# Kernel tuning notes

Hardware: AMD Instinct MI355X
Metric: run time of the kernel (lower is better)

The kernel has to match this reference:

```python
import jax, jax.numpy as jnp
import numpy as np
from jax import lax

B, S, I, H, O = 128, 1024, 512, 1024, 512


def setup_inputs() -> dict:
    key = jax.random.key(0)
    ks = jax.random.split(key, 7)
    scale_ih = 1.0 / np.sqrt(H)  # torch nn.RNN init scale
    return {
        "x": jax.random.normal(ks[0], (B, S, I), dtype=jnp.float32),
        "W_ih": jax.random.uniform(ks[1], (H, I), jnp.float32, -scale_ih, scale_ih),
        "W_hh": jax.random.uniform(ks[2], (H, H), jnp.float32, -scale_ih, scale_ih),
        "b_ih": jax.random.uniform(ks[3], (H,), jnp.float32, -scale_ih, scale_ih),
        "b_hh": jax.random.uniform(ks[4], (H,), jnp.float32, -scale_ih, scale_ih),
        "W_fc": jax.random.uniform(ks[5], (O, H), jnp.float32, -scale_ih, scale_ih),
        "b_fc": jax.random.uniform(ks[6], (O,), jnp.float32, -scale_ih, scale_ih),
    }


def reference(x, W_ih, W_hh, b_ih, b_hh, W_fc, b_fc):
    # Precompute input projections for all timesteps in one big GEMM: [B,S,H]
    xp = jnp.einsum("bsi,hi->bsh", x, W_ih) + b_ih + b_hh
    h0 = jnp.zeros((x.shape[0], W_hh.shape[0]), dtype=x.dtype)

    def step(h, xt):  # h: [B,H], xt: [B,H]
        h_new = jnp.tanh(xt + h @ W_hh.T)
        return h_new, None

    hT, _ = lax.scan(step, h0, jnp.swapaxes(xp, 0, 1))  # scan over seq dim
    # fc applied to last timestep's hidden state only
    return hT @ W_fc.T + b_fc
```

## Files before the change

### kernel.cpp

```cpp
#include <hip/hip_runtime.h>
#include <stdint.h>
#include <stddef.h>
#include <math.h>

#define B_ 128
#define S_ 1024
#define I_ 512
#define H_ 1024
#define O_ 512

typedef __attribute__((ext_vector_type(4))) float f32x4;
typedef __attribute__((ext_vector_type(8))) short short8;
typedef __attribute__((ext_vector_type(2))) unsigned int uint2v;
typedef __attribute__((ext_vector_type(4))) unsigned int uint4v;

__device__ __forceinline__ unsigned short f2bf(float f) {
    unsigned u = __builtin_bit_cast(unsigned, f);
    u += 0x7fffu + ((u >> 16) & 1u);
    return (unsigned short)(u >> 16);
}
__device__ __forceinline__ uint2v pack4(f32x4 v) {
    uint2v r;
    r.x = (unsigned)f2bf(v.x) | ((unsigned)f2bf(v.y) << 16);
    r.y = (unsigned)f2bf(v.z) | ((unsigned)f2bf(v.w) << 16);
    return r;
}
__device__ __forceinline__ unsigned long long ld_u64_coh(const unsigned long long* p) {
    return __hip_atomic_load(p, __ATOMIC_RELAXED, __HIP_MEMORY_SCOPE_AGENT);
}
__device__ __forceinline__ void st_u32_coh(unsigned int* p, unsigned int v) {
    __hip_atomic_store(p, v, __ATOMIC_RELAXED, __HIP_MEMORY_SCOPE_AGENT);
}
__device__ __forceinline__ unsigned int ld_u32_coh(const unsigned int* p) {
    return __hip_atomic_load(p, __ATOMIC_RELAXED, __HIP_MEMORY_SCOPE_AGENT);
}

#define OFF_WFI  2097152UL
#define OFF_HBUF 3145728UL
#define OFF_CNT  3670016UL
#define WS_NEED  (OFF_CNT + 2048UL)

__global__ void rnn_init(unsigned int* hb32, unsigned int* cnt) {
    int idx = blockIdx.x * 256 + threadIdx.x;
    hb32[idx] = 0u;
    hb32[idx + 65536] = 0u;
    if (blockIdx.x < 2) cnt[blockIdx.x * 256 + threadIdx.x] = 0u;
}

__global__ void rnn_convw_hh(const float* __restrict__ Whh,
                             unsigned short* __restrict__ wfh) {
    int G = blockIdx.x * 256 + threadIdx.x;
    int l = G & 63, rest = G >> 6;
    int kc = rest & 31, t = (rest >> 5) & 1, wgn = rest >> 6;
    int n  = wgn * 32 + t * 16 + (l & 15);
    int k0 = kc * 32 + (l >> 4) * 8;
    const float* src = Whh + (size_t)n * H_ + k0;
    f32x4 f0 = *(const f32x4*)src, f1 = *(const f32x4*)(src + 4);
    uint2v a = pack4(f0), b = pack4(f1);
    uint4v pk; pk.x = a.x; pk.y = a.y; pk.z = b.x; pk.w = b.y;
    *(uint4v*)(wfh + (size_t)G * 8) = pk;
}

__global__ void rnn_convw_ih(const float* __restrict__ Wih,
                             unsigned short* __restrict__ wfi) {
    int G = blockIdx.x * 256 + threadIdx.x;
    int l = G & 63, rest = G >> 6;
    int kc2 = rest & 15, t = (rest >> 4) & 1, wgn = rest >> 5;
    int n  = wgn * 32 + t * 16 + (l & 15);
    int k0 = kc2 * 32 + (l >> 4) * 8;
    const float* src = Wih + (size_t)n * I_ + k0;
    f32x4 f0 = *(const f32x4*)src, f1 = *(const f32x4*)(src + 4);
    uint2v a = pack4(f0), b = pack4(f1);
    uint4v pk; pk.x = a.x; pk.y = a.y; pk.z = b.x; pk.w = b.y;
    *(uint4v*)(wfi + (size_t)G * 8) = pk;
}

__global__ __launch_bounds__(256, 1) void rnn_rec(
    const float* __restrict__ x,
    const unsigned short* __restrict__ wfh,
    const unsigned short* __restrict__ wfi,
    const float* __restrict__ bih, const float* __restrict__ bhh,
    unsigned short* __restrict__ hbuf,
    unsigned int* __restrict__ cnt)
{
    __shared__ unsigned short ldsX[8192];
    __shared__ float red[512];

    int g = blockIdx.x & 7, wgn = blockIdx.x >> 3;
    int tid = threadIdx.x, l = tid & 63, w = tid >> 6;
    int t = w & 1, kk = w >> 1;
    int li = l & 15, q = l >> 4;

    short8 wh[16], wi[8];
    #pragma unroll
    for (int c = 0; c < 16; ++c)
        wh[c] = *(const short8*)(wfh +
            ((size_t)((wgn * 2 + t) * 32 + kk * 16 + c)) * 512 + l * 8);
    #pragma unroll
    for (int c = 0; c < 8; ++c)
        wi[c] = *(const short8*)(wfi +
            ((size_t)((wgn * 2 + t) * 16 + kk * 8 + c)) * 512 + l * 8);

    int hcol = wgn * 32 + t * 16 + li;
    float bias = 0.f;
    if (kk == 0) bias = bih[hcol] + bhh[hcol];
    int q2 = (hcol >> 3) & 3, j2 = hcol & 7;
    unsigned int* flg = cnt + g * 64;

    {
        f32x4 xr[8];
        #pragma unroll
        for (int i = 0; i < 4; ++i) {
            int G = tid + i * 256, l2 = G & 63, kc2 = G >> 6;
            const float* src = x + ((size_t)(g * 16 + (l2 & 15)) * S_ + 0) * I_
                                 + kc2 * 32 + (l2 >> 4) * 8;
            xr[2 * i]     = *(const f32x4*)src;
            xr[2 * i + 1] = *(const f32x4*)(src + 4);
        }
        #pragma unroll
        for (int i = 0; i < 4; ++i) {
            int G = tid + i * 256;
            uint2v a = pack4(xr[2 * i]), b = pack4(xr[2 * i + 1]);
            uint4v pk; pk.x = a.x; pk.y = a.y; pk.z = b.x; pk.w = b.y;
            *(uint4v*)&ldsX[(size_t)G * 8] = pk;
        }
    }
    __syncthreads();

    int bail = 0;
    #pragma unroll 1
    for (int s = 0; s < S_; ++s) {
        int cur = s & 1, nxt = cur ^ 1;
        int havex = (s + 1 < S_);

        const unsigned long long* hsrc = (const unsigned long long*)hbuf
            + (size_t)cur * 32768 + (size_t)g * 4096
            + (size_t)kk * 2048 + (size_t)l * 2;
        unsigned long long h0[16], h1[16];
        #pragma unroll
        for (int c = 0; c < 16; ++c) {
            h0[c] = ld_u64_coh(hsrc + (size_t)c * 128);
            h1[c] = ld_u64_coh(hsrc + (size_t)c * 128 + 1);
        }

        f32x4 xr[8];
        if (havex) {
            #pragma unroll
            for (int i = 0; i < 4; ++i) {
                int G = tid + i * 256, l2 = G & 63, kc2 = G >> 6;
                const float* src = x + ((size_t)(g * 16 + (l2 & 15)) * S_ + (s + 1)) * I_
                                     + kc2 * 32 + (l2 >> 4) * 8;
                xr[2 * i]     = *(const f32x4*)src;
                xr[2 * i + 1] = *(const f32x4*)(src + 4);
            }
        }

        f32x4 acc2 = {0.f, 0.f, 0.f, 0.f};
        #pragma unroll
        for (int c = 0; c < 8; ++c) {
            short8 a = *(const short8*)&ldsX[(kk * 8 + c) * 512 + l * 8];
            acc2 = __builtin_amdgcn_mfma_f32_16x16x32_bf16(a, wi[c], acc2, 0, 0, 0);
        }
        f32x4 acc = {0.f, 0.f, 0.f, 0.f};
        #pragma unroll
        for (int c = 0; c < 16; ++c) {
            union { unsigned long long qw[2]; short8 v; } u;
            u.qw[0] = h0[c]; u.qw[1] = h1[c];
            acc = __builtin_amdgcn_mfma_f32_16x16x32_bf16(u.v, wh[c], acc, 0, 0, 0);
        }
        acc += acc2;

        if (kk == 1) *(f32x4*)&red[t * 256 + l * 4] = acc;
        __syncthreads();
        if (kk == 0) {
            f32x4 p = *(const f32x4*)&red[t * 256 + l * 4];
            unsigned int* hout32 = (unsigned int*)(hbuf
                + (size_t)nxt * 131072 + (size_t)g * 16384
                + (size_t)wgn * 512 + j2);
            #pragma unroll
            for (int i = 0; i < 4; ++i) {
                float v = tanhf(acc[i] + p[i] + bias);
                unsigned short mybf = f2bf(v);
                unsigned nb = (unsigned)__shfl_xor((int)mybf, 1, 64) & 0xffffu;
                if ((li & 1) == 0) {
                    unsigned word = (unsigned)mybf | (nb << 16);
                    st_u32_coh(hout32 + (q2 * 16 + q * 4 + i) * 4, word);
                }
            }
        }
        __syncthreads();

        if (havex) {
            if (tid == 0) st_u32_coh(flg + wgn, (unsigned)(s + 1));
            #pragma unroll
            for (int i = 0; i < 4; ++i) {
                int G = tid + i * 256;
                uint2v a = pack4(xr[2 * i]), b2 = pack4(xr[2 * i + 1]);
                uint4v pk; pk.x = a.x; pk.y = a.y; pk.z = b2.x; pk.w = b2.y;
                *(uint4v*)&ldsX[(size_t)G * 8] = pk;
            }
            if (tid < 64 && !bail) {
                unsigned target = (unsigned)(s + 1);
                int polls = 0;
                while (true) {
                    unsigned v = ld_u32_coh(flg + (l & 31));
                    if (__ballot((int)(v >= target)) == ~0ull) break;
                    __builtin_amdgcn_s_sleep(1);
                    if (++polls > (1 << 22)) { bail = 1; break; }
                }
            }
            __syncthreads();
        }
    }
}

__global__ __launch_bounds__(256) void rnn_fc(
    const unsigned short* __restrict__ hb0,
    const float* __restrict__ Wfc, const float* __restrict__ bfc,
    float* __restrict__ out)
{
    __shared__ unsigned short ldsB[8 * 64 * 8];
    int n_blk = blockIdx.x;
    int tid = threadIdx.x, l = tid & 63, w = tid >> 6;
    int li = l & 15, q = l >> 4;
    f32x4 acc[8][2];
    f32x4 z = {0.f, 0.f, 0.f, 0.f};
    #pragma unroll
    for (int mb = 0; mb < 8; ++mb) { acc[mb][0] = z; acc[mb][1] = z; }

    for (int kc = 0; kc < 32; ++kc) {
        #pragma unroll
        for (int u = 0; u < 2; ++u) {
            int G = tid * 2 + u;
            int nt = G >> 6, ll = G & 63;
            int n = n_blk * 128 + nt * 16 + (ll & 15);
            int k = kc * 32 + (ll >> 4) * 8;
            const float* src = Wfc + (size_t)n * H_ + k;
            f32x4 f0 = *(const f32x4*)src, f1 = *(const f32x4*)(src + 4);
            uint2v a = pack4(f0), b = pack4(f1);
            uint4v pk; pk.x = a.x; pk.y = a.y; pk.z = b.x; pk.w = b.y;
            *(uint4v*)&ldsB[G * 8] = pk;
        }
        __syncthreads();
        short8 bfr[2];
        #pragma unroll
        for (int tn = 0; tn < 2; ++tn)
            bfr[tn] = *(const short8*)&ldsB[((w * 2 + tn) * 64 + l) * 8];
        #pragma unroll
        for (int mb = 0; mb < 8; ++mb) {
            short8 a = *(const short8*)(hb0 + (size_t)mb * 16384 + kc * 512 + l * 8);
            acc[mb][0] = __builtin_amdgcn_mfma_f32_16x16x32_bf16(a, bfr[0], acc[mb][0], 0, 0, 0);
            acc[mb][1] = __builtin_amdgcn_mfma_f32_16x16x32_bf16(a, bfr[1], acc[mb][1], 0, 0, 0);
        }
        __syncthreads();
    }
    #pragma unroll
    for (int mb = 0; mb < 8; ++mb)
        #pragma unroll
        for (int tn = 0; tn < 2; ++tn)
            #pragma unroll
            for (int i = 0; i < 4; ++i) {
                int b = mb * 16 + q * 4 + i;
                int o = n_blk * 128 + (w * 2 + tn) * 16 + li;
                out[(size_t)b * O_ + o] = acc[mb][tn][i] + bfc[o];
            }
}

extern "C" void kernel_launch(void* const* d_in, const int* in_sizes, int n_in,
                              void* d_out, int out_size, void* d_ws, size_t ws_size,
                              hipStream_t stream) {
    const float* x   = (const float*)d_in[0];
    const float* Wih = (const float*)d_in[1];
    const float* Whh = (const float*)d_in[2];
    const float* bih = (const float*)d_in[3];
    const float* bhh = (const float*)d_in[4];
    const float* Wfc = (const float*)d_in[5];
    const float* bfc = (const float*)d_in[6];
    float* out = (float*)d_out;
    (void)in_sizes; (void)n_in; (void)out_size;

    if (ws_size < WS_NEED) return;

    char* ws = (char*)d_ws;
    unsigned short* wfh  = (unsigned short*)ws;
    unsigned short* wfi  = (unsigned short*)(ws + OFF_WFI);
    unsigned short* hbuf = (unsigned short*)(ws + OFF_HBUF);
    unsigned int*   cnt  = (unsigned int*)(ws + OFF_CNT);

    rnn_init<<<256, 256, 0, stream>>>((unsigned int*)hbuf, cnt);
    rnn_convw_hh<<<512, 256, 0, stream>>>(Whh, wfh);
    rnn_convw_ih<<<256, 256, 0, stream>>>(Wih, wfi);

    const float* xa = x; const float* biha = bih; const float* bhha = bhh;
    void* args[] = {(void*)&xa, (void*)&wfh, (void*)&wfi,
                    (void*)&biha, (void*)&bhha, (void*)&hbuf, (void*)&cnt};
    hipLaunchCooperativeKernel((const void*)rnn_rec, dim3(256), dim3(256),
                               args, 0, stream);

    rnn_fc<<<4, 256, 0, stream>>>(hbuf, Wfc, bfc, out);
}
```

Measured before the change: 4.800 ms.

## Split recurrent K across four waves and add same-XCC fast sync path

Restructures the recurrent kernel so each of the four waves owns a quarter of the K dimension for both 16-column tiles, with a four-way LDS reduction replacing the previous two-way split. It detects whether all workgroups in a batch group share one XCC and, if so, uses non-temporal sc0 loads/stores with store-readback verification and per-wave flags instead of agent-scope atomics. It also swaps tanhf for an exp-based tanh, moves the next-step x prefetch after the MFMAs, and uses raw s_barrier primitives. The fast path depends on cache-coherence assumptions within an XCC and on spin-polling, which risks correctness or hangs if those assumptions fail.

After: 8.273 ms. +72.4%, slower.

```diff
diff --git a/kernel.cpp b/kernel.cpp
--- a/kernel.cpp
+++ b/kernel.cpp
@@ -14,6 +14,8 @@
 typedef __attribute__((ext_vector_type(2))) unsigned int uint2v;
 typedef __attribute__((ext_vector_type(4))) unsigned int uint4v;
 
+template <bool V> struct BC { static constexpr bool value = V; };
+
 __device__ __forceinline__ unsigned short f2bf(float f) {
     unsigned u = __builtin_bit_cast(unsigned, f);
     u += 0x7fffu + ((u >> 16) & 1u);
@@ -34,17 +36,29 @@
 __device__ __forceinline__ unsigned int ld_u32_coh(const unsigned int* p) {
     return __hip_atomic_load(p, __ATOMIC_RELAXED, __HIP_MEMORY_SCOPE_AGENT);
 }
+__device__ __forceinline__ float fast_tanh(float z) {
+    float e = __expf(2.0f * z);
+    return 1.0f - 2.0f / (e + 1.0f);
+}
+__device__ __forceinline__ void bar_lgkm() {
+    asm volatile("s_waitcnt lgkmcnt(0)\n\ts_barrier" ::: "memory");
+    __builtin_amdgcn_sched_barrier(0);
+}
+__device__ __forceinline__ void bar_only() {
+    asm volatile("s_barrier" ::: "memory");
+    __builtin_amdgcn_sched_barrier(0);
+}
 
 #define OFF_WFI  2097152UL
 #define OFF_HBUF 3145728UL
 #define OFF_CNT  3670016UL
-#define WS_NEED  (OFF_CNT + 2048UL)
+#define WS_NEED  (OFF_CNT + 4096UL)
 
 __global__ void rnn_init(unsigned int* hb32, unsigned int* cnt) {
     int idx = blockIdx.x * 256 + threadIdx.x;
     hb32[idx] = 0u;
     hb32[idx + 65536] = 0u;
-    if (blockIdx.x < 2) cnt[blockIdx.x * 256 + threadIdx.x] = 0u;
+    if (blockIdx.x < 4) cnt[blockIdx.x * 256 + threadIdx.x] = 0u;
 }
 
 __global__ void rnn_convw_hh(const float* __restrict__ Whh,
@@ -84,114 +98,69 @@
     unsigned int* __restrict__ cnt)
 {
     __shared__ unsigned short ldsX[8192];
-    __shared__ float red[512];
+    __shared__ f32x4 redv[512];
+    __shared__ int fastmode;
 
     int g = blockIdx.x & 7, wgn = blockIdx.x >> 3;
     int tid = threadIdx.x, l = tid & 63, w = tid >> 6;
-    int t = w & 1, kk = w >> 1;
     int li = l & 15, q = l >> 4;
 
-    short8 wh[16], wi[8];
+    short8 wh[2][8], wi[2][4];
     #pragma unroll
-    for (int c = 0; c < 16; ++c)
-        wh[c] = *(const short8*)(wfh +
-            ((size_t)((wgn * 2 + t) * 32 + kk * 16 + c)) * 512 + l * 8);
-    #pragma unroll
-    for (int c = 0; c < 8; ++c)
-        wi[c] = *(const short8*)(wfi +
-            ((size_t)((wgn * 2 + t) * 16 + kk * 8 + c)) * 512 + l * 8);
-
-    int hcol = wgn * 32 + t * 16 + li;
+    for (int t2 = 0; t2 < 2; ++t2) {
+        #pragma unroll
+        for (int c = 0; c < 8; ++c)
+            wh[t2][c] = *(const short8*)(wfh +
+                ((size_t)((wgn * 2 + t2) * 32 + w * 8 + c)) * 512 + l * 8);
+        #pragma unroll
+        for (int c = 0; c < 4; ++c)
+            wi[t2][c] = *(const short8*)(wfi +
+                ((size_t)((wgn * 2 + t2) * 16 + w * 4 + c)) * 512 + l * 8);
+    }
+
+    int hcol = wgn * 32 + w * 16 + li;
     float bias = 0.f;
-    if (kk == 0) bias = bih[hcol] + bhh[hcol];
+    if (w < 2) bias = bih[hcol] + bhh[hcol];
     int q2 = (hcol >> 3) & 3, j2 = hcol & 7;
     unsigned int* flg = cnt + g * 64;
 
-    {
-        f32x4 xr[8];
-        #pragma unroll
-        for (int i = 0; i < 4; ++i) {
-            int G = tid + i * 256, l2 = G & 63, kc2 = G >> 6;
-            const float* src = x + ((size_t)(g * 16 + (l2 & 15)) * S_ + 0) * I_
-                                 + kc2 * 32 + (l2 >> 4) * 8;
-            xr[2 * i]     = *(const f32x4*)src;
-            xr[2 * i + 1] = *(const f32x4*)(src + 4);
+    unsigned xcc = 0;
+    asm volatile("s_getreg_b32 %0, hwreg(HW_REG_XCC_ID)" : "=s"(xcc));
+    unsigned int* xa = cnt + 512 + g * 64;
+    if (tid == 0) st_u32_coh(xa + wgn, xcc + 1u);
+    if (tid < 64) {
+        unsigned v = 0; int polls = 0, dead = 0;
+        while (true) {
+            v = ld_u32_coh(xa + (l & 31));
+            if (__ballot((int)(v != 0u)) == ~0ull) break;
+            __builtin_amdgcn_s_sleep(1);
+            if (++polls > (1 << 22)) { dead = 1; break; }
         }
-        #pragma unroll
-        for (int i = 0; i < 4; ++i) {
-            int G = tid + i * 256;
-            uint2v a = pack4(xr[2 * i]), b = pack4(xr[2 * i + 1]);
-            uint4v pk; pk.x = a.x; pk.y = a.y; pk.z = b.x; pk.w = b.y;
-            *(uint4v*)&ldsX[(size_t)G * 8] = pk;
-        }
+        int uni = (!dead && __ballot((int)(v == xcc + 1u)) == ~0ull) ? 1 : 0;
+        if (tid == 0) fastmode = uni;
+    }
+
+    f32x4 xr[8];
+    #pragma unroll
+    for (int i = 0; i < 4; ++i) {
+        int G = tid + i * 256, l2 = G & 63, kc2 = G >> 6;
+        const float* src = x + ((size_t)(g * 16 + (l2 & 15)) * S_ + 0) * I_
+                             + kc2 * 32 + (l2 >> 4) * 8;
+        xr[2 * i]     = *(const f32x4*)src;
+        xr[2 * i + 1] = *(const f32x4*)(src + 4);
     }
     __syncthreads();
-
-    int bail = 0;
-    #pragma unroll 1
-    for (int s = 0; s < S_; ++s) {
-        int cur = s & 1, nxt = cur ^ 1;
-        int havex = (s + 1 < S_);
-
-        const unsigned long long* hsrc = (const unsigned long long*)hbuf
-            + (size_t)cur * 32768 + (size_t)g * 4096
-            + (size_t)kk * 2048 + (size_t)l * 2;
-        unsigned long long h0[16], h1[16];
-        #pragma unroll
-        for (int c = 0; c < 16; ++c) {
-            h0[c] = ld_u64_coh(hsrc + (size_t)c * 128);
-            h1[c] = ld_u64_coh(hsrc + (size_t)c * 128 + 1);
-        }
-
-        f32x4 xr[8];
-        if (havex) {
-            #pragma unroll
-            for (int i = 0; i < 4; ++i) {
-                int G = tid + i * 256, l2 = G & 63, kc2 = G >> 6;
-                const float* src = x + ((size_t)(g * 16 + (l2 & 15)) * S_ + (s + 1)) * I_
-                                     + kc2 * 32 + (l2 >> 4) * 8;
-                xr[2 * i]     = *(const f32x4*)src;
-                xr[2 * i + 1] = *(const f32x4*)(src + 4);
-            }
-        }
-
-        f32x4 acc2 = {0.f, 0.f, 0.f, 0.f};
-        #pragma unroll
-        for (int c = 0; c < 8; ++c) {
-            short8 a = *(const short8*)&ldsX[(kk * 8 + c) * 512 + l * 8];
-            acc2 = __builtin_amdgcn_mfma_f32_16x16x32_bf16(a, wi[c], acc2, 0, 0, 0);
-        }
-        f32x4 acc = {0.f, 0.f, 0.f, 0.f};
-        #pragma unroll
-        for (int c = 0; c < 16; ++c) {
-            union { unsigned long long qw[2]; short8 v; } u;
-            u.qw[0] = h0[c]; u.qw[1] = h1[c];
-            acc = __builtin_amdgcn_mfma_f32_16x16x32_bf16(u.v, wh[c], acc, 0, 0, 0);
-        }
-        acc += acc2;
-
-        if (kk == 1) *(f32x4*)&red[t * 256 + l * 4] = acc;
-        __syncthreads();
-        if (kk == 0) {
-            f32x4 p = *(const f32x4*)&red[t * 256 + l * 4];
-            unsigned int* hout32 = (unsigned int*)(hbuf
-                + (size_t)nxt * 131072 + (size_t)g * 16384
-                + (size_t)wgn * 512 + j2);
-            #pragma unroll
-            for (int i = 0; i < 4; ++i) {
-                float v = tanhf(acc[i] + p[i] + bias);
-                unsigned short mybf = f2bf(v);
-                unsigned nb = (unsigned)__shfl_xor((int)mybf, 1, 64) & 0xffffu;
-                if ((li & 1) == 0) {
-                    unsigned word = (unsigned)mybf | (nb << 16);
-                    st_u32_coh(hout32 + (q2 * 16 + q * 4 + i) * 4, word);
-                }
-            }
-        }
-        __syncthreads();
-
-        if (havex) {
-            if (tid == 0) st_u32_coh(flg + wgn, (unsigned)(s + 1));
+    const bool fast = (fastmode != 0);
+
+    auto body = [&](auto fc) {
+        constexpr bool FAST = decltype(fc)::value;
+        int bail = 0;
+        #pragma unroll 1
+        for (int s = 0; s < S_; ++s) {
+            int cur = s & 1, nxt = cur ^ 1;
+            int havex = (s + 1 < S_);
+            int sp = (s + 1) & (S_ - 1);
+
             #pragma unroll
             for (int i = 0; i < 4; ++i) {
                 int G = tid + i * 256;
@@ -199,19 +168,151 @@
                 uint4v pk; pk.x = a.x; pk.y = a.y; pk.z = b2.x; pk.w = b2.y;
                 *(uint4v*)&ldsX[(size_t)G * 8] = pk;
             }
-            if (tid < 64 && !bail) {
-                unsigned target = (unsigned)(s + 1);
-                int polls = 0;
-                while (true) {
-                    unsigned v = ld_u32_coh(flg + (l & 31));
-                    if (__ballot((int)(v >= target)) == ~0ull) break;
-                    __builtin_amdgcn_s_sleep(1);
-                    if (++polls > (1 << 22)) { bail = 1; break; }
-                }
-            }
-            __syncthreads();
+
+            uint4v hv[8];
+            unsigned long long h64a[8], h64b[8];
+            const char* hb = (const char*)hbuf + (size_t)cur * 262144
+                + (size_t)g * 32768 + (size_t)w * 8192 + (size_t)l * 16;
+            if constexpr (FAST) {
+                #pragma unroll
+                for (int c = 0; c < 8; ++c) {
+                    const char* pc = hb + c * 1024;
+                    asm volatile("global_load_dwordx4 %0, %1, off sc0 nt"
+                                 : "=&v"(hv[c]) : "v"(pc) : "memory");
+                }
+                __builtin_amdgcn_sched_barrier(0);
+            } else {
+                #pragma unroll
+                for (int c = 0; c < 8; ++c) {
+                    h64a[c] = ld_u64_coh((const unsigned long long*)(hb + c * 1024));
+                    h64b[c] = ld_u64_coh((const unsigned long long*)(hb + c * 1024 + 8));
+                }
+            }
+
+            bar_lgkm();
+
+            f32x4 a0 = {0.f, 0.f, 0.f, 0.f}, a1 = {0.f, 0.f, 0.f, 0.f};
+            #pragma unroll
+            for (int c = 0; c < 4; ++c) {
+                short8 a = *(const short8*)&ldsX[(w * 4 + c) * 512 + l * 8];
+                a0 = __builtin_amdgcn_mfma_f32_16x16x32_bf16(a, wi[0][c], a0, 0, 0, 0);
+                a1 = __builtin_amdgcn_mfma_f32_16x16x32_bf16(a, wi[1][c], a1, 0, 0, 0);
+            }
+
+            if constexpr (FAST) {
+                asm volatile("s_waitcnt vmcnt(0)" ::: "memory");
+                __builtin_amdgcn_sched_barrier(0);
+            }
+            #pragma unroll
+            for (int c = 0; c < 8; ++c) {
+                short8 af;
+                if constexpr (FAST) {
+                    af = __builtin_bit_cast(short8, hv[c]);
+                } else {
+                    union { unsigned long long qw[2]; short8 v; } uu;
+                    uu.qw[0] = h64a[c]; uu.qw[1] = h64b[c];
+                    af = uu.v;
+                }
+                a0 = __builtin_amdgcn_mfma_f32_16x16x32_bf16(af, wh[0][c], a0, 0, 0, 0);
+                a1 = __builtin_amdgcn_mfma_f32_16x16x32_bf16(af, wh[1][c], a1, 0, 0, 0);
+            }
+
+            #pragma unroll
+            for (int i = 0; i < 4; ++i) {
+                int G = tid + i * 256, l2 = G & 63, kc2 = G >> 6;
+                const float* src = x + ((size_t)(g * 16 + (l2 & 15)) * S_ + sp) * I_
+                                     + kc2 * 32 + (l2 >> 4) * 8;
+                xr[2 * i]     = *(const f32x4*)src;
+                xr[2 * i + 1] = *(const f32x4*)(src + 4);
+            }
+
+            redv[(w * 2 + 0) * 64 + l] = a0;
+            redv[(w * 2 + 1) * 64 + l] = a1;
+            bar_lgkm();
+
+            if (w < 2) {
+                f32x4 p0 = redv[(0 * 2 + w) * 64 + l];
+                f32x4 p1 = redv[(1 * 2 + w) * 64 + l];
+                f32x4 p2 = redv[(2 * 2 + w) * 64 + l];
+                f32x4 p3 = redv[(3 * 2 + w) * 64 + l];
+                unsigned int* hout32 = (unsigned int*)(hbuf
+                    + (size_t)nxt * 131072 + (size_t)g * 16384
+                    + (size_t)wgn * 512 + j2);
+                unsigned wv0 = 0, wv1 = 0, wv2 = 0, wv3 = 0;
+                unsigned int *dp0 = 0, *dp1 = 0, *dp2 = 0, *dp3 = 0;
+                #pragma unroll
+                for (int i = 0; i < 4; ++i) {
+                    float z = p0[i] + p1[i] + p2[i] + p3[i] + bias;
+                    float v = fast_tanh(z);
+                    unsigned short mybf = f2bf(v);
+                    unsigned nb = (unsigned)__shfl_xor((int)mybf, 1, 64) & 0xffffu;
+                    unsigned word = (unsigned)mybf | (nb << 16);
+                    unsigned int* dst = hout32 + (q2 * 16 + q * 4 + i) * 4;
+                    if ((li & 1) == 0) {
+                        if constexpr (FAST) *(volatile unsigned int*)dst = word;
+                        else st_u32_coh(dst, word);
+                    }
+                    if (i == 0) { wv0 = word; dp0 = dst; }
+                    else if (i == 1) { wv1 = word; dp1 = dst; }
+                    else if (i == 2) { wv2 = word; dp2 = dst; }
+                    else { wv3 = word; dp3 = dst; }
+                }
+                if constexpr (FAST) {
+                    if ((li & 1) == 0) {
+                        int tries = 0;
+                        while (true) {
+                            unsigned g0, g1, g2, g3;
+                            asm volatile(
+                                "global_load_dword %0, %4, off sc0 nt\n\t"
+                                "global_load_dword %1, %5, off sc0 nt\n\t"
+                                "global_load_dword %2, %6, off sc0 nt\n\t"
+                                "global_load_dword %3, %7, off sc0 nt\n\t"
+                                "s_waitcnt vmcnt(0)"
+                                : "=&v"(g0), "=&v"(g1), "=&v"(g2), "=&v"(g3)
+                                : "v"(dp0), "v"(dp1), "v"(dp2), "v"(dp3)
+                                : "memory");
+                            if (g0 == wv0 && g1 == wv1 && g2 == wv2 && g3 == wv3) break;
+                            if (++tries > (1 << 20)) break;
+                        }
+                    }
+                    __builtin_amdgcn_sched_barrier(0);
+                } else {
+                    asm volatile("s_waitcnt vmcnt(0)" ::: "memory");
+                    __builtin_amdgcn_sched_barrier(0);
+                }
+                if (l == 0) {
+                    if constexpr (FAST)
+                        *(volatile unsigned int*)(flg + w * 32 + wgn) = (unsigned)(s + 1);
+                    else
+                        st_u32_coh(flg + w * 32 + wgn, (unsigned)(s + 1));
+                }
+            }
+
+            if (havex) {
+                if (w == 0 && !bail) {
+                    unsigned target = (unsigned)(s + 1);
+                    int polls = 0;
+                    while (true) {
+                        unsigned v2;
+                        if constexpr (FAST) {
+                            asm volatile(
+                                "global_load_dword %0, %1, off sc0 nt\n\t"
+                                "s_waitcnt vmcnt(0)"
+                                : "=&v"(v2) : "v"(flg + l) : "memory");
+                        } else {
+                            v2 = ld_u32_coh(flg + l);
+                        }
+                        if (__ballot((int)(v2 >= target)) == ~0ull) break;
+                        __builtin_amdgcn_s_sleep(1);
+                        if (++polls > (1 << 22)) { bail = 1; break; }
+                    }
+                }
+                bar_only();
+            }
         }
-    }
+    };
+    if (fast) body(BC<true>{});
+    else      body(BC<false>{});
 }
 
 __global__ __launch_bounds__(256) void rnn_fc(
```
